# Kernel tuning notes

Measured on AMD Instinct MI355X. Metric: run time of the kernel, lower is better.

## Reference

```python
import jax, jax.numpy as jnp
import numpy as np
from jax.ops import segment_sum

N0 = 50000
N1 = 50000
E = 300000
D = 128
L = 3
EPS_GIN = 0.1
COEF = 0.1
BN_EPS = 1e-5


def setup_inputs() -> dict:
    key = jax.random.key(0)
    ks = jax.random.split(key, 32)
    inp = {}
    inp['x0'] = jax.random.randint(ks[0], (N0, 2), 0, 3)
    inp['x1'] = jax.random.randint(ks[1], (N1, 2), 0, 3)
    inp['ei101'] = jax.random.randint(ks[2], (2, E), 0, N1)
    inp['ea101'] = jax.random.randint(ks[3], (E, 2), 0, 3)
    inp['ei110'] = jax.random.randint(ks[4], (2, E), 0, N0)  # src '1' -> dst '0' (N1==N0)
    inp['ea110'] = jax.random.randint(ks[5], (E, 2), 0, 3)
    inp['ei021'] = jax.random.randint(ks[6], (2, E), 0, N1)  # src '0' -> dst '1'
    inp['ea021'] = jax.random.randint(ks[7], (E, 2), 0, 3)
    inp['ei030'] = jax.random.randint(ks[8], (2, E), 0, N0)
    inp['ea030'] = jax.random.randint(ks[9], (E, 2), 0, 3)
    # learned parameters
    s = 0.05
    inp['x_emb1'] = jax.random.normal(ks[10], (120, D), jnp.float32) * s
    inp['x_emb2'] = jax.random.normal(ks[11], (3, D), jnp.float32) * s
    inp['e_emb1'] = jax.random.normal(ks[12], (6, D), jnp.float32) * s
    inp['e_emb2'] = jax.random.normal(ks[13], (3, D), jnp.float32) * s
    w = 1.0 / np.sqrt(D)
    inp['gin_w1'] = jax.random.normal(ks[14], (D, 2 * D), jnp.float32) * w
    inp['gin_b1'] = jnp.zeros((2 * D,), jnp.float32)
    inp['gin_w2'] = jax.random.normal(ks[15], (2 * D, D), jnp.float32) * (1.0 / np.sqrt(2 * D))
    inp['gin_b2'] = jnp.zeros((D,), jnp.float32)
    inp['w110'] = jax.random.normal(ks[16], (D, D), jnp.float32) * w
    inp['b110'] = jnp.zeros((D,), jnp.float32)
    inp['w021'] = jax.random.normal(ks[17], (D, D), jnp.float32) * w
    inp['b021'] = jnp.zeros((D,), jnp.float32)
    inp['w030'] = jax.random.normal(ks[18], (D, D), jnp.float32) * w
    inp['b030'] = jnp.zeros((D,), jnp.float32)
    inp['bn_gamma'] = jnp.ones((L, D), jnp.float32)
    inp['bn_beta'] = jnp.zeros((L, D), jnp.float32)
    return inp


def _add_self_loops(ei, ea, n):
    loop = jnp.arange(n, dtype=ei.dtype)
    ei = jnp.concatenate([ei, jnp.stack([loop, loop])], axis=1)
    self_attr = jnp.tile(jnp.array([[4, 0]], dtype=ea.dtype), (n, 1))
    return ei, jnp.concatenate([ea, self_attr], axis=0)


def _bn(x, gamma, beta):
    # training-mode BatchNorm1d: batch statistics, biased variance
    mu = jnp.mean(x, axis=0)
    var = jnp.var(x, axis=0)
    return (x - mu) * jax.lax.rsqrt(var + BN_EPS) * gamma + beta


def reference(x0, x1, ei101, ea101, ei110, ea110, ei021, ea021, ei030, ea030,
              x_emb1, x_emb2, e_emb1, e_emb2,
              gin_w1, gin_b1, gin_w2, gin_b2,
              w110, b110, w021, b021, w030, b030,
              bn_gamma, bn_beta):
    n0, n1 = x0.shape[0], x1.shape[0]
    # AddSelfLoops only for homogeneous edge types, fill_value=[4,0]
    ei101, ea101 = _add_self_loops(ei101, ea101, n1)
    ei030, ea030 = _add_self_loops(ei030, ea030, n0)

    h0 = x_emb1[x0[:, 0]] + x_emb2[x0[:, 1]]
    h1 = x_emb1[x1[:, 0]] + x_emb2[x1[:, 1]]
    e101 = e_emb1[ea101[:, 0]] + e_emb2[ea101[:, 1]]
    e110 = e_emb1[ea110[:, 0]] + e_emb2[ea110[:, 1]]
    e021 = e_emb1[ea021[:, 0]] + e_emb2[ea021[:, 1]]
    e030 = e_emb1[ea030[:, 0]] + e_emb2[ea030[:, 1]]

    def gin(h_src, h_dst, ei, eattr):
        agg = segment_sum(h_src[ei[0]] + eattr, ei[1], num_segments=h_dst.shape[0])
        z = agg + (1.0 + EPS_GIN) * h_dst
        return jnp.maximum(z @ gin_w1 + gin_b1, 0.0) @ gin_w2 + gin_b2

    def lin(h_src, n_dst, ei, eattr, w, b):
        agg = segment_sum(h_src[ei[0]] + eattr, ei[1], num_segments=n_dst)
        return (agg @ w + b) * COEF

    for layer in range(L):
        # HeteroConv aggr='mean' over convs sharing a destination node type
        out1 = 0.5 * (gin(h1, h1, ei101, e101) + lin(h0, n1, ei021, e021, w021, b021))
        out0 = 0.5 * (lin(h1, n0, ei110, e110, w110, b110) + lin(h0, n0, ei030, e030, w030, b030))
        g, b = bn_gamma[layer], bn_beta[layer]
        h0, h1 = _bn(out0, g, b), _bn(out1, g, b)
        if layer < L - 1:
            h0, h1 = jax.nn.relu(h0), jax.nn.relu(h1)
    # to_homogeneous().x: node types in order '0', '1'
    return jnp.concatenate([h0, h1], axis=0)
```

## Files before the change

### kernel.cpp

```cpp
#include <hip/hip_runtime.h>

#define D 128
#define BN_EPS 1e-5f
#define MAXNB 16

typedef __attribute__((ext_vector_type(8))) short bf16x8;
typedef __attribute__((ext_vector_type(4))) float f32x4;

__device__ __forceinline__ unsigned short f2bf(float x) {
  unsigned u = __float_as_uint(x);
  u += 0x7FFF + ((u >> 16) & 1);
  return (unsigned short)(u >> 16);
}
__device__ __forceinline__ float bf2f(unsigned short u) {
  return __uint_as_float((unsigned)u << 16);
}

__global__ __launch_bounds__(256) void k_etbl(const float* __restrict__ e1,
                                              const float* __restrict__ e2,
                                              float* __restrict__ etbl) {
  int idx = blockIdx.x * 256 + threadIdx.x;
  if (idx < 9 * D) {
    int combo = idx / D, c = idx % D;
    etbl[idx] = e1[(combo / 3) * D + c] + e2[(combo % 3) * D + c];
  } else if (idx < 10 * D) {
    int c = idx - 9 * D;
    etbl[idx] = e1[4 * D + c] + e2[c];
  }
}

__global__ __launch_bounds__(256) void k_embed(const int* __restrict__ x,
                                               const float* __restrict__ emb1,
                                               const float* __restrict__ emb2,
                                               unsigned short* __restrict__ out,
                                               int n) {
  int idx = blockIdx.x * 256 + threadIdx.x;
  if (idx >= n * 32) return;
  int node = idx >> 5, c4 = idx & 31;
  int i1 = x[2 * node], i2 = x[2 * node + 1];
  float4 v1 = *(const float4*)(emb1 + (size_t)i1 * D + c4 * 4);
  float4 v2 = *(const float4*)(emb2 + (size_t)i2 * D + c4 * 4);
  ushort4 o;
  o.x = f2bf(v1.x + v2.x); o.y = f2bf(v1.y + v2.y);
  o.z = f2bf(v1.z + v2.z); o.w = f2bf(v1.w + v2.w);
  *(ushort4*)(out + (size_t)node * D + c4 * 4) = o;
}

__global__ __launch_bounds__(256) void k_wprep(const float* __restrict__ W,
                                               unsigned short* __restrict__ Wt,
                                               int K, int N, float scale) {
  int idx = blockIdx.x * 256 + threadIdx.x;
  if (idx >= K * N) return;
  int n = idx / K, k = idx - n * K;
  Wt[idx] = f2bf(W[(size_t)k * N + n] * scale);
}

__global__ __launch_bounds__(256) void k_bprep(
    const float* __restrict__ b110, const float* __restrict__ b030,
    const float* __restrict__ gb1, const float* __restrict__ gb2,
    const float* __restrict__ b021, float* __restrict__ bias0,
    float* __restrict__ biash, float* __restrict__ bias1) {
  int i = threadIdx.x;
  if (i < 128) {
    bias0[i] = 0.05f * (b110[i] + b030[i]);
    bias1[i] = 0.5f * gb2[i] + 0.05f * b021[i];
  }
  biash[i] = gb1[i];
}

struct EdgeArr {
  const int* ei[4];
  const int* ea[4];
  int* cur[4];
  int* pay[4];
};
struct CsrPtrs {
  int* cur[4];
  int* rp[4];
  int n[4];
};

__global__ __launch_bounds__(256) void k_hist4(EdgeArr A, int E) {
  int t = blockIdx.y;
  int e = blockIdx.x * 256 + threadIdx.x;
  if (e >= E) return;
  atomicAdd(&A.cur[t][A.ei[t][E + e]], 1);
}

__global__ __launch_bounds__(256) void k_scan1(CsrPtrs p, int* __restrict__ bsum) {
  __shared__ int lds[256];
  int type = blockIdx.y;
  const int* cur = p.cur[type];
  int n = p.n[type];
  int base = blockIdx.x * 4096;
  int s = 0;
  for (int i = threadIdx.x; i < 4096; i += 256) {
    int idx = base + i;
    if (idx < n) s += cur[idx];
  }
  int tid = threadIdx.x;
  lds[tid] = s;
  __syncthreads();
  for (int off = 128; off > 0; off >>= 1) {
    if (tid < off) lds[tid] += lds[tid + off];
    __syncthreads();
  }
  if (tid == 0) bsum[type * MAXNB + blockIdx.x] = lds[0];
}

__global__ __launch_bounds__(64) void k_scan2(int* __restrict__ bsum) {
  int t = threadIdx.x;
  if (t < 4) {
    int run = 0;
    for (int i = 0; i < MAXNB; ++i) {
      int v = bsum[t * MAXNB + i];
      bsum[t * MAXNB + i] = run;
      run += v;
    }
  }
}

__global__ __launch_bounds__(256) void k_scan3(CsrPtrs p,
                                               const int* __restrict__ bsum,
                                               int E) {
  __shared__ int lds[256];
  int type = blockIdx.y;
  int* cur = p.cur[type];
  int* rp = p.rp[type];
  int n = p.n[type];
  int tid = threadIdx.x;
  if (blockIdx.x == 0 && tid == 0) rp[n] = E;
  int t0 = blockIdx.x * 4096 + tid * 16;
  int loc[16];
  int s = 0;
#pragma unroll
  for (int j = 0; j < 16; ++j) {
    int idx = t0 + j;
    int v = (idx < n) ? cur[idx] : 0;
    loc[j] = s;
    s += v;
  }
  lds[tid] = s;
  __syncthreads();
  for (int off = 1; off < 256; off <<= 1) {
    int v = (tid >= off) ? lds[tid - off] : 0;
    __syncthreads();
    lds[tid] += v;
    __syncthreads();
  }
  int off0 = bsum[type * MAXNB + blockIdx.x] + ((tid == 0) ? 0 : lds[tid - 1]);
#pragma unroll
  for (int j = 0; j < 16; ++j) {
    int idx = t0 + j;
    if (idx < n) {
      int v = off0 + loc[j];
      rp[idx] = v;
      cur[idx] = v;
    }
  }
}

__global__ __launch_bounds__(256) void k_fill4(EdgeArr A, int E) {
  int t = blockIdx.y;
  int e = blockIdx.x * 256 + threadIdx.x;
  if (e >= E) return;
  const int* ei = A.ei[t];
  const int* ea = A.ea[t];
  int dst = ei[E + e];
  int src = ei[e];
  int combo = ea[2 * e] * 3 + ea[2 * e + 1];
  int pos = atomicAdd(&A.cur[t][dst], 1);
  A.pay[t][pos] = src | (combo << 16);
}

template <int MODE, bool NORM>
__global__ __launch_bounds__(256) void k_gather(
    const unsigned short* __restrict__ hsrc,
    const unsigned short* __restrict__ hinit, const int* __restrict__ rowptr,
    const int* __restrict__ payload, const float* __restrict__ etbl,
    const float* __restrict__ bnp, unsigned short* __restrict__ agg, int n) {
  __shared__ float et[10 * D];
  for (int i = threadIdx.x; i < 10 * D; i += 256) et[i] = etbl[i];
  __syncthreads();
  int g = blockIdx.x * 8 + (threadIdx.x >> 5);
  if (g >= n) return;
  int l = threadIdx.x & 31;
  int c = l * 4;
  float4 scv, shv;
  if (NORM) {
    scv = *(const float4*)(bnp + c);
    shv = *(const float4*)(bnp + D + c);
  }

  auto xform = [&](ushort4 hv) {
    float4 r;
    r.x = bf2f(hv.x); r.y = bf2f(hv.y); r.z = bf2f(hv.z); r.w = bf2f(hv.w);
    if (NORM) {
      r.x = fmaxf(fmaf(r.x, scv.x, shv.x), 0.f);
      r.y = fmaxf(fmaf(r.y, scv.y, shv.y), 0.f);
      r.z = fmaxf(fmaf(r.z, scv.z, shv.z), 0.f);
      r.w = fmaxf(fmaf(r.w, scv.w, shv.w), 0.f);
    }
    return r;
  };
  auto fetch = [&](int p) {
    int src = p & 0xFFFF;
    int combo = p >> 16;
    float4 h = xform(*(const ushort4*)(hsrc + (size_t)src * D + c));
    float4 r;
    r.x = h.x + et[combo * D + c + 0];
    r.y = h.y + et[combo * D + c + 1];
    r.z = h.z + et[combo * D + c + 2];
    r.w = h.w + et[combo * D + c + 3];
    return r;
  };

  float4 acc, acc2 = make_float4(0.f, 0.f, 0.f, 0.f);
  if (MODE == 0) {
    acc = make_float4(0.f, 0.f, 0.f, 0.f);
  } else {
    float4 h = xform(*(const ushort4*)(hinit + (size_t)g * D + c));
    float sc = (MODE == 2) ? 2.1f : 1.0f;
    acc.x = sc * h.x + et[9 * D + c + 0];
    acc.y = sc * h.y + et[9 * D + c + 1];
    acc.z = sc * h.z + et[9 * D + c + 2];
    acc.w = sc * h.w + et[9 * D + c + 3];
  }

  int e0 = rowptr[g], e1 = rowptr[g + 1];
  int e = e0;
  while (e < e1) {
    int cnt = min(32, e1 - e);
    int pv = (e + l < e1) ? payload[e + l] : 0;
    int j = 0;
    for (; j + 1 < cnt; j += 2) {
      int p0 = __shfl(pv, j, 32);
      int p1 = __shfl(pv, j + 1, 32);
      float4 t0 = fetch(p0);
      float4 t1 = fetch(p1);
      acc.x += t0.x; acc.y += t0.y; acc.z += t0.z; acc.w += t0.w;
      acc2.x += t1.x; acc2.y += t1.y; acc2.z += t1.z; acc2.w += t1.w;
    }
    if (j < cnt) {
      float4 t = fetch(__shfl(pv, j, 32));
      acc.x += t.x; acc.y += t.y; acc.z += t.z; acc.w += t.w;
    }
    e += cnt;
  }
  acc.x += acc2.x; acc.y += acc2.y; acc.z += acc2.z; acc.w += acc2.w;
  ushort4 o;
  o.x = f2bf(acc.x); o.y = f2bf(acc.y); o.z = f2bf(acc.z); o.w = f2bf(acc.w);
  *(ushort4*)(agg + (size_t)g * D + c) = o;
}

template <int NCOLS, int K1, int K2, bool RELU, bool STATS, bool OBF16>
__global__ __launch_bounds__(256) void gemm_breg(
    const unsigned short* __restrict__ A1, const unsigned short* __restrict__ Wt1,
    const unsigned short* __restrict__ A2, const unsigned short* __restrict__ Wt2,
    const float* __restrict__ bias, void* __restrict__ Cv, int M,
    float* __restrict__ stats) {
  constexpr int WC = NCOLS / 4;
  constexpr int CF = WC / 16;
  constexpr int KF1 = K1 / 32;
  constexpr int KF2 = (K2 > 0) ? (K2 / 32) : 1;

  int tid = threadIdx.x;
  int w = tid >> 6, l = tid & 63;
  int lr = l & 15, lk = l >> 4;
  int colbase = w * WC;
  int row0 = blockIdx.x * 64;

  f32x4 acc[4][CF];
#pragma unroll
  for (int rf = 0; rf < 4; ++rf)
#pragma unroll
    for (int cf = 0; cf < CF; ++cf) acc[rf][cf] = (f32x4)(0.f);

  {
    const unsigned short* ap[4];
#pragma unroll
    for (int rf = 0; rf < 4; ++rf) {
      int r = row0 + rf * 16 + lr;
      if (r > M - 1) r = M - 1;
      ap[rf] = A1 + (size_t)r * K1 + lk * 8;
    }
    bf16x8 B[CF][KF1];
#pragma unroll
    for (int cf = 0; cf < CF; ++cf)
#pragma unroll
      for (int kf = 0; kf < KF1; ++kf)
        B[cf][kf] = *(const bf16x8*)(Wt1 + (size_t)(colbase + cf * 16 + lr) * K1 +
                                     kf * 32 + lk * 8);
#pragma unroll
    for (int kf = 0; kf < KF1; ++kf) {
      bf16x8 a[4];
#pragma unroll
      for (int rf = 0; rf < 4; ++rf) a[rf] = *(const bf16x8*)(ap[rf] + kf * 32);
#pragma unroll
      for (int rf = 0; rf < 4; ++rf)
#pragma unroll
        for (int cf = 0; cf < CF; ++cf)
          acc[rf][cf] = __builtin_amdgcn_mfma_f32_16x16x32_bf16(a[rf], B[cf][kf],
                                                                acc[rf][cf], 0, 0, 0);
    }
  }
  if constexpr (K2 > 0) {
    const unsigned short* ap[4];
#pragma unroll
    for (int rf = 0; rf < 4; ++rf) {
      int r = row0 + rf * 16 + lr;
      if (r > M - 1) r = M - 1;
      ap[rf] = A2 + (size_t)r * K2 + lk * 8;
    }
    bf16x8 B[CF][KF2];
#pragma unroll
    for (int cf = 0; cf < CF; ++cf)
#pragma unroll
      for (int kf = 0; kf < KF2; ++kf)
        B[cf][kf] = *(const bf16x8*)(Wt2 + (size_t)(colbase + cf * 16 + lr) * K2 +
                                     kf * 32 + lk * 8);
#pragma unroll
    for (int kf = 0; kf < KF2; ++kf) {
      bf16x8 a[4];
#pragma unroll
      for (int rf = 0; rf < 4; ++rf) a[rf] = *(const bf16x8*)(ap[rf] + kf * 32);
#pragma unroll
      for (int rf = 0; rf < 4; ++rf)
#pragma unroll
        for (int cf = 0; cf < CF; ++cf)
          acc[rf][cf] = __builtin_amdgcn_mfma_f32_16x16x32_bf16(a[rf], B[cf][kf],
                                                                acc[rf][cf], 0, 0, 0);
    }
  }

  float bv[CF];
#pragma unroll
  for (int cf = 0; cf < CF; ++cf) bv[cf] = bias[colbase + cf * 16 + lr];

  float colS[CF], colQ[CF];
#pragma unroll
  for (int cf = 0; cf < CF; ++cf) { colS[cf] = 0.f; colQ[cf] = 0.f; }

  float* Cf = (float*)Cv;
  unsigned short* Cb = (unsigned short*)Cv;
#pragma unroll
  for (int rf = 0; rf < 4; ++rf) {
#pragma unroll
    for (int r = 0; r < 4; ++r) {
      int row = row0 + rf * 16 + lk * 4 + r;
      bool ok = row < M;
#pragma unroll
      for (int cf = 0; cf < CF; ++cf) {
        int col = colbase + cf * 16 + lr;
        float v = acc[rf][cf][r] + bv[cf];
        if (RELU) v = fmaxf(v, 0.f);
        if (ok) {
          if (OBF16)
            Cb[(size_t)row * NCOLS + col] = f2bf(v);
          else
            Cf[(size_t)row * NCOLS + col] = v;
          if (STATS) { colS[cf] += v; colQ[cf] += v * v; }
        }
      }
    }
  }

  if constexpr (STATS) {
#pragma unroll
    for (int cf = 0; cf < CF; ++cf) {
      float s = colS[cf], q = colQ[cf];
      s += __shfl_xor(s, 16); q += __shfl_xor(q, 16);
      s += __shfl_xor(s, 32); q += __shfl_xor(q, 32);
      if (lk == 0) {
        int col = colbase + cf * 16 + lr;
        atomicAdd(&stats[col], s);
        atomicAdd(&stats[D + col], q);
      }
    }
  }
}

__global__ __launch_bounds__(256) void k_bnprep(const float* __restrict__ stats,
                                                const float* __restrict__ gamma,
                                                const float* __restrict__ beta,
                                                float* __restrict__ bnp0,
                                                float* __restrict__ bnp1,
                                                float invM0, float invM1) {
  int i = threadIdx.x;
  if (i < 128) {
    float mu = stats[i] * invM0;
    float var = stats[D + i] * invM0 - mu * mu;
    float sc = rsqrtf(var + BN_EPS) * gamma[i];
    bnp0[i] = sc;
    bnp0[D + i] = beta[i] - mu * sc;
  } else {
    int d = i - 128;
    float mu = stats[2 * D + d] * invM1;
    float var = stats[3 * D + d] * invM1 - mu * mu;
    float sc = rsqrtf(var + BN_EPS) * gamma[d];
    bnp1[d] = sc;
    bnp1[D + d] = beta[d] - mu * sc;
  }
}

__global__ __launch_bounds__(256) void k_bnfin(float* __restrict__ X, int M,
                                               const float* __restrict__ bnp) {
  int idx = blockIdx.x * 256 + threadIdx.x;
  int i = idx >> 5, c4 = idx & 31;
  if (i >= M) return;
  float4 v = *(float4*)(X + (size_t)i * D + c4 * 4);
  float4 sc = *(const float4*)(bnp + c4 * 4);
  float4 sh = *(const float4*)(bnp + D + c4 * 4);
  float4 o;
  o.x = fmaf(v.x, sc.x, sh.x); o.y = fmaf(v.y, sc.y, sh.y);
  o.z = fmaf(v.z, sc.z, sh.z); o.w = fmaf(v.w, sc.w, sh.w);
  *(float4*)(X + (size_t)i * D + c4 * 4) = o;
}

extern "C" void kernel_launch(void* const* d_in, const int* in_sizes, int n_in,
                              void* d_out, int out_size, void* d_ws,
                              size_t ws_size, hipStream_t stream) {
  const int* x0 = (const int*)d_in[0];
  const int* x1 = (const int*)d_in[1];
  const int* ei101 = (const int*)d_in[2];
  const int* ea101 = (const int*)d_in[3];
  const int* ei110 = (const int*)d_in[4];
  const int* ea110 = (const int*)d_in[5];
  const int* ei021 = (const int*)d_in[6];
  const int* ea021 = (const int*)d_in[7];
  const int* ei030 = (const int*)d_in[8];
  const int* ea030 = (const int*)d_in[9];
  const float* x_emb1 = (const float*)d_in[10];
  const float* x_emb2 = (const float*)d_in[11];
  const float* e_emb1 = (const float*)d_in[12];
  const float* e_emb2 = (const float*)d_in[13];
  const float* gin_w1 = (const float*)d_in[14];
  const float* gin_b1 = (const float*)d_in[15];
  const float* gin_w2 = (const float*)d_in[16];
  const float* gin_b2 = (const float*)d_in[17];
  const float* w110 = (const float*)d_in[18];
  const float* b110 = (const float*)d_in[19];
  const float* w021 = (const float*)d_in[20];
  const float* b021 = (const float*)d_in[21];
  const float* w030 = (const float*)d_in[22];
  const float* b030 = (const float*)d_in[23];
  const float* bn_gamma = (const float*)d_in[24];
  const float* bn_beta = (const float*)d_in[25];

  int n0 = in_sizes[0] / 2, n1 = in_sizes[1] / 2;
  int E = in_sizes[2] / 2;
  int nmax = n0 > n1 ? n0 : n1;

  float* h0f = (float*)d_out;
  float* h1f = h0f + (size_t)n0 * D;

  char* p = (char*)d_ws;
  auto alloc = [&](size_t bytes) {
    char* r = p;
    p += (bytes + 63) & ~(size_t)63;
    return r;
  };
  unsigned short* h0r = (unsigned short*)alloc((size_t)n0 * D * 2);
  unsigned short* h1r = (unsigned short*)alloc((size_t)n1 * D * 2);
  unsigned short* z1b = (unsigned short*)alloc((size_t)n1 * D * 2);
  unsigned short* a021b = (unsigned short*)alloc((size_t)n1 * D * 2);
  unsigned short* a110b = (unsigned short*)alloc((size_t)n0 * D * 2);
  unsigned short* a030b = (unsigned short*)alloc((size_t)n0 * D * 2);
  unsigned short* hiddenb = (unsigned short*)alloc((size_t)n1 * 256 * 2);
  float* etbl = (float*)alloc(10 * D * 4);
  float* stats = (float*)alloc(4 * D * 4);
  float* bnp0 = (float*)alloc(2 * D * 4);
  float* bnp1 = (float*)alloc(2 * D * 4);
  unsigned short* wt110 = (unsigned short*)alloc(128 * 128 * 2);
  unsigned short* wt030 = (unsigned short*)alloc(128 * 128 * 2);
  unsigned short* wt021 = (unsigned short*)alloc(128 * 128 * 2);
  unsigned short* wtg1 = (unsigned short*)alloc(256 * 128 * 2);
  unsigned short* wtg2 = (unsigned short*)alloc(128 * 256 * 2);
  float* bias0 = (float*)alloc(128 * 4);
  float* biash = (float*)alloc(256 * 4);
  float* bias1 = (float*)alloc(128 * 4);

  EdgeArr EA;
  CsrPtrs cp;
  const int* eis[4] = {ei101, ei021, ei110, ei030};
  const int* eas[4] = {ea101, ea021, ea110, ea030};
  int ndst[4] = {n1, n1, n0, n0};
  for (int t = 0; t < 4; ++t) {
    cp.rp[t] = (int*)alloc((size_t)(nmax + 1) * 4);
    cp.cur[t] = (int*)alloc((size_t)nmax * 4);
    EA.pay[t] = (int*)alloc((size_t)E * 4);
    cp.n[t] = ndst[t];
    EA.ei[t] = eis[t];
    EA.ea[t] = eas[t];
    EA.cur[t] = cp.cur[t];
  }
  int* bsum = (int*)alloc(4 * MAXNB * 4);

  dim3 b256(256);
  int eBlocks = (E + 255) / 256;

  k_etbl<<<5, b256, 0, stream>>>(e_emb1, e_emb2, etbl);
  k_embed<<<(n0 * 32 + 255) / 256, b256, 0, stream>>>(x0, x_emb1, x_emb2, h0r, n0);
  k_embed<<<(n1 * 32 + 255) / 256, b256, 0, stream>>>(x1, x_emb1, x_emb2, h1r, n1);
  k_wprep<<<64, b256, 0, stream>>>(w110, wt110, 128, 128, 0.05f);
  k_wprep<<<64, b256, 0, stream>>>(w030, wt030, 128, 128, 0.05f);
  k_wprep<<<64, b256, 0, stream>>>(w021, wt021, 128, 128, 0.05f);
  k_wprep<<<128, b256, 0, stream>>>(gin_w1, wtg1, 128, 256, 1.0f);
  k_wprep<<<128, b256, 0, stream>>>(gin_w2, wtg2, 256, 128, 0.5f);
  k_bprep<<<1, b256, 0, stream>>>(b110, b030, gin_b1, gin_b2, b021, bias0, biash, bias1);

  for (int t = 0; t < 4; ++t)
    hipMemsetAsync(cp.cur[t], 0, (size_t)ndst[t] * sizeof(int), stream);
  k_hist4<<<dim3(eBlocks, 4), b256, 0, stream>>>(EA, E);
  hipMemsetAsync(bsum, 0, 4 * MAXNB * sizeof(int), stream);
  int nb = (nmax + 4095) / 4096;
  k_scan1<<<dim3(nb, 4), b256, 0, stream>>>(cp, bsum);
  k_scan2<<<1, dim3(64), 0, stream>>>(bsum);
  k_scan3<<<dim3(nb, 4), b256, 0, stream>>>(cp, bsum, E);
  k_fill4<<<dim3(eBlocks, 4), b256, 0, stream>>>(EA, E);

  int gB0 = (n0 + 7) / 8, gB1 = (n1 + 7) / 8;
  int mB0 = (n0 + 63) / 64, mB1 = (n1 + 63) / 64;

  for (int layer = 0; layer < 3; ++layer) {
    if (layer == 0) {
      k_gather<2, false><<<gB1, b256, 0, stream>>>(h1r, h1r, cp.rp[0], EA.pay[0], etbl, nullptr, z1b, n1);
      k_gather<0, false><<<gB1, b256, 0, stream>>>(h0r, nullptr, cp.rp[1], EA.pay[1], etbl, nullptr, a021b, n1);
      k_gather<0, false><<<gB0, b256, 0, stream>>>(h1r, nullptr, cp.rp[2], EA.pay[2], etbl, nullptr, a110b, n0);
      k_gather<1, false><<<gB0, b256, 0, stream>>>(h0r, h0r, cp.rp[3], EA.pay[3], etbl, nullptr, a030b, n0);
    } else {
      k_gather<2, true><<<gB1, b256, 0, stream>>>(h1r, h1r, cp.rp[0], EA.pay[0], etbl, bnp1, z1b, n1);
      k_gather<0, true><<<gB1, b256, 0, stream>>>(h0r, nullptr, cp.rp[1], EA.pay[1], etbl, bnp0, a021b, n1);
      k_gather<0, true><<<gB0, b256, 0, stream>>>(h1r, nullptr, cp.rp[2], EA.pay[2], etbl, bnp1, a110b, n0);
      k_gather<1, true><<<gB0, b256, 0, stream>>>(h0r, h0r, cp.rp[3], EA.pay[3], etbl, bnp0, a030b, n0);
    }

    hipMemsetAsync(stats, 0, 4 * D * sizeof(float), stream);

    if (layer < 2) {
      gemm_breg<128, 128, 128, false, true, true><<<mB0, b256, 0, stream>>>(
          a110b, wt110, a030b, wt030, bias0, h0r, n0, stats);
      gemm_breg<256, 128, 0, true, false, true><<<mB1, b256, 0, stream>>>(
          z1b, wtg1, nullptr, nullptr, biash, hiddenb, n1, nullptr);
      gemm_breg<128, 256, 128, false, true, true><<<mB1, b256, 0, stream>>>(
          hiddenb, wtg2, a021b, wt021, bias1, h1r, n1, stats + 2 * D);
    } else {
      gemm_breg<128, 128, 128, false, true, false><<<mB0, b256, 0, stream>>>(
          a110b, wt110, a030b, wt030, bias0, h0f, n0, stats);
      gemm_breg<256, 128, 0, true, false, true><<<mB1, b256, 0, stream>>>(
          z1b, wtg1, nullptr, nullptr, biash, hiddenb, n1, nullptr);
      gemm_breg<128, 256, 128, false, true, false><<<mB1, b256, 0, stream>>>(
          hiddenb, wtg2, a021b, wt021, bias1, h1f, n1, stats + 2 * D);
    }

    k_bnprep<<<1, b256, 0, stream>>>(stats, bn_gamma + layer * D,
                                     bn_beta + layer * D, bnp0, bnp1,
                                     1.0f / n0, 1.0f / n1);
    if (layer == 2) {
      k_bnfin<<<(n0 * 32 + 255) / 256, b256, 0, stream>>>(h0f, n0, bnp0);
      k_bnfin<<<(n1 * 32 + 255) / 256, b256, 0, stream>>>(h1f, n1, bnp1);
    }
  }
}
```

Baseline: 797.0 us.

## Merge four gather launches into one batched kernel with 16-byte row loads

Replaces the four per-edge-type gather launches per layer with a single launch that uses blockIdx.y to select the edge type. Each node is now handled by 16 lanes loading 8 bf16 values (16 bytes) each, instead of 32 lanes loading 4, and the edge loop is unrolled by four so more independent row loads are in flight. This cuts launch overhead and improves memory-level parallelism. The cost is that mode and norm become runtime branches rather than template parameters, and each lane holds more registers.

```diff
diff --git a/kernel.cpp b/kernel.cpp
--- a/kernel.cpp
+++ b/kernel.cpp
@@ -173,84 +173,119 @@
   A.pay[t][pos] = src | (combo << 16);
 }
 
-template <int MODE, bool NORM>
-__global__ __launch_bounds__(256) void k_gather(
-    const unsigned short* __restrict__ hsrc,
-    const unsigned short* __restrict__ hinit, const int* __restrict__ rowptr,
-    const int* __restrict__ payload, const float* __restrict__ etbl,
-    const float* __restrict__ bnp, unsigned short* __restrict__ agg, int n) {
+struct GArgs {
+  const unsigned short* src[4];
+  const unsigned short* ini[4];
+  const float* bnp[4];
+  const int* rp[4];
+  const int* pay[4];
+  unsigned short* agg[4];
+  int mode[4];
+  int n[4];
+  int norm;
+};
+
+__device__ __forceinline__ void cvt8(float (&f)[8], bf16x8 r) {
+  const unsigned* u = (const unsigned*)&r;
+#pragma unroll
+  for (int j = 0; j < 4; ++j) {
+    f[2 * j] = __uint_as_float(u[j] << 16);
+    f[2 * j + 1] = __uint_as_float(u[j] & 0xFFFF0000u);
+  }
+}
+
+__device__ __forceinline__ void addrow(float (&acc)[8], bf16x8 r,
+                                       const float* etp, const float (&sc)[8],
+                                       const float (&sh)[8], bool norm) {
+  float f[8];
+  cvt8(f, r);
+  if (norm) {
+#pragma unroll
+    for (int j = 0; j < 8; ++j) f[j] = fmaxf(fmaf(f[j], sc[j], sh[j]), 0.f);
+  }
+  float4 ea = *(const float4*)etp;
+  float4 eb = *(const float4*)(etp + 4);
+  acc[0] += f[0] + ea.x; acc[1] += f[1] + ea.y;
+  acc[2] += f[2] + ea.z; acc[3] += f[3] + ea.w;
+  acc[4] += f[4] + eb.x; acc[5] += f[5] + eb.y;
+  acc[6] += f[6] + eb.z; acc[7] += f[7] + eb.w;
+}
+
+__global__ __launch_bounds__(256) void k_gather_all(GArgs G,
+                                                    const float* __restrict__ etbl) {
   __shared__ float et[10 * D];
   for (int i = threadIdx.x; i < 10 * D; i += 256) et[i] = etbl[i];
   __syncthreads();
-  int g = blockIdx.x * 8 + (threadIdx.x >> 5);
-  if (g >= n) return;
-  int l = threadIdx.x & 31;
-  int c = l * 4;
-  float4 scv, shv;
-  if (NORM) {
-    scv = *(const float4*)(bnp + c);
-    shv = *(const float4*)(bnp + D + c);
-  }
-
-  auto xform = [&](ushort4 hv) {
-    float4 r;
-    r.x = bf2f(hv.x); r.y = bf2f(hv.y); r.z = bf2f(hv.z); r.w = bf2f(hv.w);
-    if (NORM) {
-      r.x = fmaxf(fmaf(r.x, scv.x, shv.x), 0.f);
-      r.y = fmaxf(fmaf(r.y, scv.y, shv.y), 0.f);
-      r.z = fmaxf(fmaf(r.z, scv.z, shv.z), 0.f);
-      r.w = fmaxf(fmaf(r.w, scv.w, shv.w), 0.f);
-    }
-    return r;
-  };
-  auto fetch = [&](int p) {
-    int src = p & 0xFFFF;
-    int combo = p >> 16;
-    float4 h = xform(*(const ushort4*)(hsrc + (size_t)src * D + c));
-    float4 r;
-    r.x = h.x + et[combo * D + c + 0];
-    r.y = h.y + et[combo * D + c + 1];
-    r.z = h.z + et[combo * D + c + 2];
-    r.w = h.w + et[combo * D + c + 3];
-    return r;
-  };
-
-  float4 acc, acc2 = make_float4(0.f, 0.f, 0.f, 0.f);
-  if (MODE == 0) {
-    acc = make_float4(0.f, 0.f, 0.f, 0.f);
+  int t = blockIdx.y;
+  int g = blockIdx.x * 16 + (threadIdx.x >> 4);
+  if (g >= G.n[t]) return;
+  int l = threadIdx.x & 15;
+  int c = l * 8;
+  const unsigned short* __restrict__ hsrc = G.src[t];
+  const int* __restrict__ pay = G.pay[t];
+  bool norm = G.norm != 0;
+
+  float sc[8], sh[8];
+  if (norm) {
+    const float* bnp = G.bnp[t];
+#pragma unroll
+    for (int j = 0; j < 8; ++j) { sc[j] = bnp[c + j]; sh[j] = bnp[D + c + j]; }
   } else {
-    float4 h = xform(*(const ushort4*)(hinit + (size_t)g * D + c));
-    float sc = (MODE == 2) ? 2.1f : 1.0f;
-    acc.x = sc * h.x + et[9 * D + c + 0];
-    acc.y = sc * h.y + et[9 * D + c + 1];
-    acc.z = sc * h.z + et[9 * D + c + 2];
-    acc.w = sc * h.w + et[9 * D + c + 3];
-  }
-
-  int e0 = rowptr[g], e1 = rowptr[g + 1];
+#pragma unroll
+    for (int j = 0; j < 8; ++j) { sc[j] = 1.f; sh[j] = 0.f; }
+  }
+
+  float acc[8];
+  int mode = G.mode[t];
+  if (mode == 0) {
+#pragma unroll
+    for (int j = 0; j < 8; ++j) acc[j] = 0.f;
+  } else {
+    bf16x8 hv = *(const bf16x8*)(G.ini[t] + (size_t)g * D + c);
+    float f[8];
+    cvt8(f, hv);
+    if (norm) {
+#pragma unroll
+      for (int j = 0; j < 8; ++j) f[j] = fmaxf(fmaf(f[j], sc[j], sh[j]), 0.f);
+    }
+    float m = (mode == 2) ? 2.1f : 1.0f;
+#pragma unroll
+    for (int j = 0; j < 8; ++j) acc[j] = m * f[j] + et[9 * D + c + j];
+  }
+
+  int e0 = G.rp[t][g], e1 = G.rp[t][g + 1];
   int e = e0;
   while (e < e1) {
-    int cnt = min(32, e1 - e);
-    int pv = (e + l < e1) ? payload[e + l] : 0;
+    int cnt = min(16, e1 - e);
+    int pv = (e + l < e1) ? pay[e + l] : 0;
     int j = 0;
-    for (; j + 1 < cnt; j += 2) {
-      int p0 = __shfl(pv, j, 32);
-      int p1 = __shfl(pv, j + 1, 32);
-      float4 t0 = fetch(p0);
-      float4 t1 = fetch(p1);
-      acc.x += t0.x; acc.y += t0.y; acc.z += t0.z; acc.w += t0.w;
-      acc2.x += t1.x; acc2.y += t1.y; acc2.z += t1.z; acc2.w += t1.w;
-    }
-    if (j < cnt) {
-      float4 t = fetch(__shfl(pv, j, 32));
-      acc.x += t.x; acc.y += t.y; acc.z += t.z; acc.w += t.w;
+    for (; j + 3 < cnt; j += 4) {
+      int p0 = __shfl(pv, j, 16);
+      int p1 = __shfl(pv, j + 1, 16);
+      int p2 = __shfl(pv, j + 2, 16);
+      int p3 = __shfl(pv, j + 3, 16);
+      bf16x8 r0 = *(const bf16x8*)(hsrc + (size_t)(p0 & 0xFFFF) * D + c);
+      bf16x8 r1 = *(const bf16x8*)(hsrc + (size_t)(p1 & 0xFFFF) * D + c);
+      bf16x8 r2 = *(const bf16x8*)(hsrc + (size_t)(p2 & 0xFFFF) * D + c);
+      bf16x8 r3 = *(const bf16x8*)(hsrc + (size_t)(p3 & 0xFFFF) * D + c);
+      addrow(acc, r0, et + (p0 >> 16) * D + c, sc, sh, norm);
+      addrow(acc, r1, et + (p1 >> 16) * D + c, sc, sh, norm);
+      addrow(acc, r2, et + (p2 >> 16) * D + c, sc, sh, norm);
+      addrow(acc, r3, et + (p3 >> 16) * D + c, sc, sh, norm);
+    }
+    for (; j < cnt; ++j) {
+      int p0 = __shfl(pv, j, 16);
+      bf16x8 r0 = *(const bf16x8*)(hsrc + (size_t)(p0 & 0xFFFF) * D + c);
+      addrow(acc, r0, et + (p0 >> 16) * D + c, sc, sh, norm);
     }
     e += cnt;
   }
-  acc.x += acc2.x; acc.y += acc2.y; acc.z += acc2.z; acc.w += acc2.w;
-  ushort4 o;
-  o.x = f2bf(acc.x); o.y = f2bf(acc.y); o.z = f2bf(acc.z); o.w = f2bf(acc.w);
-  *(ushort4*)(agg + (size_t)g * D + c) = o;
+
+  unsigned o0 = (unsigned)f2bf(acc[0]) | ((unsigned)f2bf(acc[1]) << 16);
+  unsigned o1 = (unsigned)f2bf(acc[2]) | ((unsigned)f2bf(acc[3]) << 16);
+  unsigned o2 = (unsigned)f2bf(acc[4]) | ((unsigned)f2bf(acc[5]) << 16);
+  unsigned o3 = (unsigned)f2bf(acc[6]) | ((unsigned)f2bf(acc[7]) << 16);
+  *(uint4*)(G.agg[t] + (size_t)g * D + c) = make_uint4(o0, o1, o2, o3);
 }
 
 template <int NCOLS, int K1, int K2, bool RELU, bool STATS, bool OBF16>
@@ -519,21 +554,22 @@
   k_scan3<<<dim3(nb, 4), b256, 0, stream>>>(cp, bsum, E);
   k_fill4<<<dim3(eBlocks, 4), b256, 0, stream>>>(EA, E);
 
-  int gB0 = (n0 + 7) / 8, gB1 = (n1 + 7) / 8;
+  GArgs GA;
+  GA.src[0] = h1r; GA.ini[0] = h1r;     GA.bnp[0] = bnp1; GA.agg[0] = z1b;   GA.mode[0] = 2; GA.n[0] = n1;
+  GA.src[1] = h0r; GA.ini[1] = nullptr; GA.bnp[1] = bnp0; GA.agg[1] = a021b; GA.mode[1] = 0; GA.n[1] = n1;
+  GA.src[2] = h1r; GA.ini[2] = nullptr; GA.bnp[2] = bnp1; GA.agg[2] = a110b; GA.mode[2] = 0; GA.n[2] = n0;
+  GA.src[3] = h0r; GA.ini[3] = h0r;     GA.bnp[3] = bnp0; GA.agg[3] = a030b; GA.mode[3] = 1; GA.n[3] = n0;
+  for (int t = 0; t < 4; ++t) {
+    GA.rp[t] = cp.rp[t];
+    GA.pay[t] = EA.pay[t];
+  }
+
   int mB0 = (n0 + 63) / 64, mB1 = (n1 + 63) / 64;
+  dim3 gGrid((nmax + 15) / 16, 4);
 
   for (int layer = 0; layer < 3; ++layer) {
-    if (layer == 0) {
-      k_gather<2, false><<<gB1, b256, 0, stream>>>(h1r, h1r, cp.rp[0], EA.pay[0], etbl, nullptr, z1b, n1);
-      k_gather<0, false><<<gB1, b256, 0, stream>>>(h0r, nullptr, cp.rp[1], EA.pay[1], etbl, nullptr, a021b, n1);
-      k_gather<0, false><<<gB0, b256, 0, stream>>>(h1r, nullptr, cp.rp[2], EA.pay[2], etbl, nullptr, a110b, n0);
-      k_gather<1, false><<<gB0, b256, 0, stream>>>(h0r, h0r, cp.rp[3], EA.pay[3], etbl, nullptr, a030b, n0);
-    } else {
-      k_gather<2, true><<<gB1, b256, 0, stream>>>(h1r, h1r, cp.rp[0], EA.pay[0], etbl, bnp1, z1b, n1);
-      k_gather<0, true><<<gB1, b256, 0, stream>>>(h0r, nullptr, cp.rp[1], EA.pay[1], etbl, bnp0, a021b, n1);
-      k_gather<0, true><<<gB0, b256, 0, stream>>>(h1r, nullptr, cp.rp[2], EA.pay[2], etbl, bnp1, a110b, n0);
-      k_gather<1, true><<<gB0, b256, 0, stream>>>(h0r, h0r, cp.rp[3], EA.pay[3], etbl, bnp0, a030b, n0);
-    }
+    GA.norm = (layer > 0) ? 1 : 0;
+    k_gather_all<<<gGrid, b256, 0, stream>>>(GA, etbl);
 
     hipMemsetAsync(stats, 0, 4 * D * sizeof(float), stream);
 
```

Result: faster. 780.2 us (-2.1%).
